# Performance work log

Measured on AMD Instinct MI355X. Metric: run time of the kernel, lower is better.

## Reference

```python
import jax, jax.numpy as jnp
import numpy as np


def setup_inputs() -> dict:
    key = jax.random.key(0)
    k1, k2 = jax.random.split(key)
    B, C, L, K = 128, 64, 4096, 31
    inputData = jax.random.normal(k1, (B, C, L), dtype=jnp.float32)
    # independentChannels=False: kernel = randn(1, C, K) expanded to (C, C, K)
    kernel = jnp.broadcast_to(jax.random.normal(k2, (1, C, K), dtype=jnp.float32), (C, C, K))
    return {"inputData": inputData, "kernel": kernel}


def reference(inputData, kernel):
    B, C, L = inputData.shape
    K = kernel.shape[-1]
    N = L + K - 1          # paddedSequenceLength
    pad = (K - 1) // 2
    # rfft with n=N zero-pads the last dim automatically (norm='backward' is jnp default)
    fourierData = jnp.fft.rfft(inputData, n=N, axis=-1)          # [B, C, N//2+1] complex
    kernelFFT = jnp.fft.rfft(kernel, n=N, axis=-1)               # [C, C, N//2+1] complex
    convFourier = jnp.einsum('oif,bif->bof', kernelFFT, fourierData)
    convData = jnp.fft.irfft(convFourier, n=N, axis=-1)          # [B, C, N]
    return convData[:, :, pad:N - pad]                           # [B, C, L]
```

## Files before the change

kernel.cpp:

```cpp
#include <hip/hip_runtime.h>

#define BATCH 128
#define C 64
#define L 4096
#define K 31

#define NT 512
#define NWAVE 8
#define CG 16
#define CPB (C / CG)
#define RW 8
#define WTILE 512

typedef float floatx4 __attribute__((ext_vector_type(4)));

__device__ __forceinline__ floatx4 ld4(const float* p) {
    return *reinterpret_cast<const floatx4*>(p);
}

#define KSTEP(k) { const float wk = wp[k];                              \
    P[(k)+0] += wk * o0.x; P[(k)+1] += wk * o0.y;                       \
    P[(k)+2] += wk * o0.z; P[(k)+3] += wk * o0.w;                       \
    P[(k)+4] += wk * o1.x; P[(k)+5] += wk * o1.y;                       \
    P[(k)+6] += wk * o1.z; P[(k)+7] += wk * o1.w; }

__global__ __launch_bounds__(NT, 2)
void computeS_kernel(const float* __restrict__ x,
                     const float* __restrict__ w,
                     float* __restrict__ Sp) {
    __shared__ float exL1[NWAVE][8];
    __shared__ float exL2a[NWAVE][8];
    __shared__ float exL2b[NWAVE][8];
    __shared__ float exR1[NWAVE][8];
    __shared__ float exR2a[NWAVE][8];
    __shared__ float exR2b[NWAVE][8];

    const int tid  = threadIdx.x;
    const int wv   = tid >> 6;
    const int lane = tid & 63;
    const int b    = blockIdx.x;
    const int cg   = blockIdx.y;
    const int l0   = wv * WTILE + lane * RW;
    const int i0   = cg * CPB;
    const float* xb = x + (long)b * C * L;

    float P[38] = {};

    const float* xi = xb + (long)i0 * L + l0;
    floatx4 o0 = ld4(xi), o1 = ld4(xi + 4);

    for (int c = 0; c < CPB; ++c) {
        floatx4 n0 = o0, n1 = o1;
        if (c + 1 < CPB) { n0 = ld4(xi + L); n1 = ld4(xi + L + 4); }

        const float* wp = w + (i0 + c) * K;
        KSTEP(0)  KSTEP(1)  KSTEP(2)  KSTEP(3)  KSTEP(4)  KSTEP(5)
        KSTEP(6)  KSTEP(7)  KSTEP(8)  KSTEP(9)  KSTEP(10) KSTEP(11)
        KSTEP(12) KSTEP(13) KSTEP(14) KSTEP(15) KSTEP(16) KSTEP(17)
        KSTEP(18) KSTEP(19) KSTEP(20) KSTEP(21) KSTEP(22) KSTEP(23)
        KSTEP(24) KSTEP(25) KSTEP(26) KSTEP(27) KSTEP(28) KSTEP(29)
        KSTEP(30)

        o0 = n0; o1 = n1;
        xi += L;
    }

    if (lane == 63) {
#pragma unroll
        for (int j = 0; j < 8; ++j) exL1[wv][j] = P[23 + j];
#pragma unroll
        for (int j = 0; j < 7; ++j) exL2b[wv][j] = P[31 + j];
    }
    if (lane == 62) {
#pragma unroll
        for (int j = 0; j < 7; ++j) exL2a[wv][j] = P[31 + j];
    }
    if (lane == 0) {
#pragma unroll
        for (int j = 0; j < 8; ++j) exR1[wv][j] = P[7 + j];
#pragma unroll
        for (int j = 0; j < 7; ++j) exR2b[wv][j] = P[j];
    }
    if (lane == 1) {
#pragma unroll
        for (int j = 0; j < 7; ++j) exR2a[wv][j] = P[j];
    }
    __syncthreads();

    float res[RW];
#pragma unroll
    for (int r = 0; r < RW; ++r) res[r] = P[15 + r];

#pragma unroll
    for (int r = 0; r < 8; ++r) {
        float v = __shfl_up(P[23 + r], 1, 64);
        if (lane == 0) v = (wv > 0) ? exL1[wv - 1][r] : 0.f;
        res[r] += v;
    }
#pragma unroll
    for (int r = 0; r < 7; ++r) {
        float v = __shfl_up(P[31 + r], 2, 64);
        if (lane == 0)      v = (wv > 0) ? exL2a[wv - 1][r] : 0.f;
        else if (lane == 1) v = (wv > 0) ? exL2b[wv - 1][r] : 0.f;
        res[r] += v;
    }
#pragma unroll
    for (int r = 0; r < 8; ++r) {
        float v = __shfl_down(P[7 + r], 1, 64);
        if (lane == 63) v = (wv < NWAVE - 1) ? exR1[wv + 1][r] : 0.f;
        res[r] += v;
    }
#pragma unroll
    for (int r = 1; r < 8; ++r) {
        float v = __shfl_down(P[r - 1], 2, 64);
        if (lane == 63)      v = (wv < NWAVE - 1) ? exR2a[wv + 1][r - 1] : 0.f;
        else if (lane == 62) v = (wv < NWAVE - 1) ? exR2b[wv + 1][r - 1] : 0.f;
        res[r] += v;
    }

    floatx4 s0, s1;
    s0.x = res[0]; s0.y = res[1]; s0.z = res[2]; s0.w = res[3];
    s1.x = res[4]; s1.y = res[5]; s1.z = res[6]; s1.w = res[7];
    float* sp = Sp + ((long)cg * BATCH + b) * L + l0;
    *reinterpret_cast<floatx4*>(sp)     = s0;
    *reinterpret_cast<floatx4*>(sp + 4) = s1;
}

__global__ __launch_bounds__(256)
void broadcast_kernel(const float* __restrict__ Sp,
                      float* __restrict__ out) {
    const int lane = threadIdx.x & 63;
    const int og   = threadIdx.x >> 6;
    const int b    = blockIdx.y;
    const int l4   = blockIdx.x * 64 + lane;
    const long sbase = (long)b * L + (long)l4 * 4;

    floatx4 v = *reinterpret_cast<const floatx4*>(Sp + sbase);
#pragma unroll
    for (int cg = 1; cg < CG; ++cg)
        v += *reinterpret_cast<const floatx4*>(Sp + (long)cg * BATCH * L + sbase);

    float* ob = out + ((long)b * C + og * 16) * L + (long)l4 * 4;
#pragma unroll
    for (int o = 0; o < 16; ++o)
        __builtin_nontemporal_store(v, reinterpret_cast<floatx4*>(ob + (long)o * L));
}

#define FB_R 4
#define FB_TILE (256 * FB_R)
#define FB_WIN 36
__global__ __launch_bounds__(256)
void fused_kernel(const float* __restrict__ x,
                  const float* __restrict__ w,
                  float* __restrict__ out) {
    const int tid = threadIdx.x;
    const int tile = blockIdx.x;
    const int b = blockIdx.y;
    const int l0 = tile * FB_TILE + tid * FB_R;
    float acc[FB_R] = {0.f, 0.f, 0.f, 0.f};
    const float* xb = x + (long)b * C * L;
    const bool interior = (l0 >= 16) && (l0 + 20 <= L);
    if (interior) {
        const float* xw = xb + (l0 - 16);
#pragma unroll 2
        for (int i = 0; i < C; ++i) {
            float win[FB_WIN];
            const floatx4* p = reinterpret_cast<const floatx4*>(xw + (long)i * L);
#pragma unroll
            for (int j = 0; j < FB_WIN / 4; ++j)
                reinterpret_cast<floatx4*>(win)[j] = p[j];
            const float* wp = w + i * K;
#pragma unroll
            for (int k = 0; k < K; ++k) {
                const float wk = wp[k];
#pragma unroll
                for (int r = 0; r < FB_R; ++r)
                    acc[r] += wk * win[r + 31 - k];
            }
        }
    } else {
        for (int i = 0; i < C; ++i) {
            const float* xi = xb + (long)i * L;
            float win[FB_WIN];
#pragma unroll
            for (int j = 0; j < FB_WIN; ++j) {
                const int g = l0 - 16 + j;
                win[j] = (g >= 0 && g < L) ? xi[g] : 0.f;
            }
            const float* wp = w + i * K;
#pragma unroll
            for (int k = 0; k < K; ++k) {
                const float wk = wp[k];
#pragma unroll
                for (int r = 0; r < FB_R; ++r)
                    acc[r] += wk * win[r + 31 - k];
            }
        }
    }
    float* op = out + (long)b * C * L + l0;
    floatx4 v; v.x = acc[0]; v.y = acc[1]; v.z = acc[2]; v.w = acc[3];
#pragma unroll
    for (int o = 0; o < C; ++o)
        __builtin_nontemporal_store(v, reinterpret_cast<floatx4*>(op + (long)o * L));
}

extern "C" void kernel_launch(void* const* d_in, const int* in_sizes, int n_in,
                              void* d_out, int out_size, void* d_ws, size_t ws_size,
                              hipStream_t stream) {
    const float* x = (const float*)d_in[0];
    const float* w = (const float*)d_in[1];
    float* out = (float*)d_out;

    const size_t sp_bytes = (size_t)CG * BATCH * L * sizeof(float);
    if (ws_size >= sp_bytes) {
        float* Sp = (float*)d_ws;
        dim3 grid1(BATCH, CG);
        computeS_kernel<<<grid1, NT, 0, stream>>>(x, w, Sp);
        dim3 grid2(L / 256, BATCH);
        broadcast_kernel<<<grid2, 256, 0, stream>>>(Sp, out);
    } else {
        dim3 grid(L / FB_TILE, BATCH);
        fused_kernel<<<grid, 256, 0, stream>>>(x, w, out);
    }
}
```

Before: 65.95 us.

## Fuse channel-sum and output broadcast into a single tiled reverse-conv kernel

Replaces the two-kernel path (partial sums written to workspace, then a reduce-and-broadcast kernel) with one kernel. Each block covers a 2048-wide sequence tile and splits the 64 input channels across two wave halves, reducing them through shared memory. Halo contributions at tile edges are computed by single lanes, and each wave writes 8 output channels straight from shared memory. This removes the workspace write/read round trip and one launch, at the cost of fewer blocks (256) and serial halo work on one lane.

```diff
diff --git a/kernel.cpp b/kernel.cpp
--- a/kernel.cpp
+++ b/kernel.cpp
@@ -7,10 +7,11 @@
 
 #define NT 512
 #define NWAVE 8
-#define CG 16
-#define CPB (C / CG)
+#define NWT 4
+#define CH 32
 #define RW 8
 #define WTILE 512
+#define BTILE 2048
 
 typedef float floatx4 __attribute__((ext_vector_type(4)));
 
@@ -25,23 +26,28 @@
     P[(k)+6] += wk * o1.z; P[(k)+7] += wk * o1.w; }
 
 __global__ __launch_bounds__(NT, 2)
-void computeS_kernel(const float* __restrict__ x,
-                     const float* __restrict__ w,
-                     float* __restrict__ Sp) {
+void revconv_fused(const float* __restrict__ x,
+                   const float* __restrict__ w,
+                   float* __restrict__ out) {
     __shared__ float exL1[NWAVE][8];
     __shared__ float exL2a[NWAVE][8];
     __shared__ float exL2b[NWAVE][8];
     __shared__ float exR1[NWAVE][8];
     __shared__ float exR2a[NWAVE][8];
     __shared__ float exR2b[NWAVE][8];
+    __shared__ __align__(16) float rbuf[BTILE];
+    __shared__ __align__(16) float sbuf[BTILE];
 
     const int tid  = threadIdx.x;
     const int wv   = tid >> 6;
     const int lane = tid & 63;
-    const int b    = blockIdx.x;
-    const int cg   = blockIdx.y;
-    const int l0   = wv * WTILE + lane * RW;
-    const int i0   = cg * CPB;
+    const int wt   = wv >> 1;
+    const int half = wv & 1;
+    const int tile = blockIdx.x;
+    const int b    = blockIdx.y;
+    const int T0   = tile * BTILE;
+    const int l0   = T0 + wt * WTILE + lane * RW;
+    const int i0   = half * CH;
     const float* xb = x + (long)b * C * L;
 
     float P[38] = {};
@@ -49,9 +55,9 @@
     const float* xi = xb + (long)i0 * L + l0;
     floatx4 o0 = ld4(xi), o1 = ld4(xi + 4);
 
-    for (int c = 0; c < CPB; ++c) {
+    for (int c = 0; c < CH; ++c) {
         floatx4 n0 = o0, n1 = o1;
-        if (c + 1 < CPB) { n0 = ld4(xi + L); n1 = ld4(xi + L + 4); }
+        if (c + 1 < CH) { n0 = ld4(xi + L); n1 = ld4(xi + L + 4); }
 
         const float* wp = w + (i0 + c) * K;
         KSTEP(0)  KSTEP(1)  KSTEP(2)  KSTEP(3)  KSTEP(4)  KSTEP(5)
@@ -65,6 +71,37 @@
         xi += L;
     }
 
+    if (wt == 0 && lane == 0 && tile > 0) {
+        for (int c = 0; c < CH; ++c) {
+            const float* gp = xb + (long)(i0 + c) * L + T0 - 16;
+            float g[16];
+#pragma unroll
+            for (int q = 0; q < 4; ++q)
+                *reinterpret_cast<floatx4*>(&g[q * 4]) = ld4(gp + q * 4);
+            const float* wp = w + (i0 + c) * K;
+#pragma unroll
+            for (int j = 1; j < 16; ++j)
+#pragma unroll
+                for (int k = 31 - j; k < 31; ++k)
+                    P[j + k - 16] += wp[k] * g[j];
+        }
+    }
+    if (wt == NWT - 1 && lane == 63 && tile == 0) {
+        for (int c = 0; c < CH; ++c) {
+            const float* gp = xb + (long)(i0 + c) * L + T0 + BTILE;
+            float g[16];
+#pragma unroll
+            for (int q = 0; q < 4; ++q)
+                *reinterpret_cast<floatx4*>(&g[q * 4]) = ld4(gp + q * 4);
+            const float* wp = w + (i0 + c) * K;
+#pragma unroll
+            for (int j = 0; j < 15; ++j)
+#pragma unroll
+                for (int k = 0; k <= 14 - j; ++k)
+                    P[j + k + 8] += wp[k] * g[j];
+        }
+    }
+
     if (lane == 63) {
 #pragma unroll
         for (int j = 0; j < 8; ++j) exL1[wv][j] = P[23 + j];
@@ -94,114 +131,61 @@
 #pragma unroll
     for (int r = 0; r < 8; ++r) {
         float v = __shfl_up(P[23 + r], 1, 64);
-        if (lane == 0) v = (wv > 0) ? exL1[wv - 1][r] : 0.f;
+        if (lane == 0) v = (wt > 0) ? exL1[wv - 2][r] : 0.f;
         res[r] += v;
     }
 #pragma unroll
     for (int r = 0; r < 7; ++r) {
         float v = __shfl_up(P[31 + r], 2, 64);
-        if (lane == 0)      v = (wv > 0) ? exL2a[wv - 1][r] : 0.f;
-        else if (lane == 1) v = (wv > 0) ? exL2b[wv - 1][r] : 0.f;
+        if (lane == 0)      v = (wt > 0) ? exL2a[wv - 2][r] : 0.f;
+        else if (lane == 1) v = (wt > 0) ? exL2b[wv - 2][r] : 0.f;
         res[r] += v;
     }
 #pragma unroll
     for (int r = 0; r < 8; ++r) {
         float v = __shfl_down(P[7 + r], 1, 64);
-        if (lane == 63) v = (wv < NWAVE - 1) ? exR1[wv + 1][r] : 0.f;
+        if (lane == 63) v = (wt < NWT - 1) ? exR1[wv + 2][r] : 0.f;
         res[r] += v;
     }
 #pragma unroll
     for (int r = 1; r < 8; ++r) {
         float v = __shfl_down(P[r - 1], 2, 64);
-        if (lane == 63)      v = (wv < NWAVE - 1) ? exR2a[wv + 1][r - 1] : 0.f;
-        else if (lane == 62) v = (wv < NWAVE - 1) ? exR2b[wv + 1][r - 1] : 0.f;
-        res[r] += v;
-    }
-
-    floatx4 s0, s1;
-    s0.x = res[0]; s0.y = res[1]; s0.z = res[2]; s0.w = res[3];
-    s1.x = res[4]; s1.y = res[5]; s1.z = res[6]; s1.w = res[7];
-    float* sp = Sp + ((long)cg * BATCH + b) * L + l0;
-    *reinterpret_cast<floatx4*>(sp)     = s0;
-    *reinterpret_cast<floatx4*>(sp + 4) = s1;
-}
-
-__global__ __launch_bounds__(256)
-void broadcast_kernel(const float* __restrict__ Sp,
-                      float* __restrict__ out) {
-    const int lane = threadIdx.x & 63;
-    const int og   = threadIdx.x >> 6;
-    const int b    = blockIdx.y;
-    const int l4   = blockIdx.x * 64 + lane;
-    const long sbase = (long)b * L + (long)l4 * 4;
-
-    floatx4 v = *reinterpret_cast<const floatx4*>(Sp + sbase);
-#pragma unroll
-    for (int cg = 1; cg < CG; ++cg)
-        v += *reinterpret_cast<const floatx4*>(Sp + (long)cg * BATCH * L + sbase);
-
-    float* ob = out + ((long)b * C + og * 16) * L + (long)l4 * 4;
-#pragma unroll
-    for (int o = 0; o < 16; ++o)
-        __builtin_nontemporal_store(v, reinterpret_cast<floatx4*>(ob + (long)o * L));
-}
-
-#define FB_R 4
-#define FB_TILE (256 * FB_R)
-#define FB_WIN 36
-__global__ __launch_bounds__(256)
-void fused_kernel(const float* __restrict__ x,
-                  const float* __restrict__ w,
-                  float* __restrict__ out) {
-    const int tid = threadIdx.x;
-    const int tile = blockIdx.x;
-    const int b = blockIdx.y;
-    const int l0 = tile * FB_TILE + tid * FB_R;
-    float acc[FB_R] = {0.f, 0.f, 0.f, 0.f};
-    const float* xb = x + (long)b * C * L;
-    const bool interior = (l0 >= 16) && (l0 + 20 <= L);
-    if (interior) {
-        const float* xw = xb + (l0 - 16);
-#pragma unroll 2
-        for (int i = 0; i < C; ++i) {
-            float win[FB_WIN];
-            const floatx4* p = reinterpret_cast<const floatx4*>(xw + (long)i * L);
-#pragma unroll
-            for (int j = 0; j < FB_WIN / 4; ++j)
-                reinterpret_cast<floatx4*>(win)[j] = p[j];
-            const float* wp = w + i * K;
-#pragma unroll
-            for (int k = 0; k < K; ++k) {
-                const float wk = wp[k];
-#pragma unroll
-                for (int r = 0; r < FB_R; ++r)
-                    acc[r] += wk * win[r + 31 - k];
-            }
+        if (lane == 63)      v = (wt < NWT - 1) ? exR2a[wv + 2][r - 1] : 0.f;
+        else if (lane == 62) v = (wt < NWT - 1) ? exR2b[wv + 2][r - 1] : 0.f;
+        res[r] += v;
+    }
+
+    const int toff = wt * WTILE + lane * RW;
+    if (half == 1) {
+        floatx4 a0, a1;
+        a0.x = res[0]; a0.y = res[1]; a0.z = res[2]; a0.w = res[3];
+        a1.x = res[4]; a1.y = res[5]; a1.z = res[6]; a1.w = res[7];
+        *reinterpret_cast<floatx4*>(&rbuf[toff])     = a0;
+        *reinterpret_cast<floatx4*>(&rbuf[toff + 4]) = a1;
+    }
+    __syncthreads();
+    if (half == 0) {
+        floatx4 s0, s1;
+        s0.x = res[0] + rbuf[toff];     s0.y = res[1] + rbuf[toff + 1];
+        s0.z = res[2] + rbuf[toff + 2]; s0.w = res[3] + rbuf[toff + 3];
+        s1.x = res[4] + rbuf[toff + 4]; s1.y = res[5] + rbuf[toff + 5];
+        s1.z = res[6] + rbuf[toff + 6]; s1.w = res[7] + rbuf[toff + 7];
+        *reinterpret_cast<floatx4*>(&sbuf[toff])     = s0;
+        *reinterpret_cast<floatx4*>(&sbuf[toff + 4]) = s1;
+    }
+    __syncthreads();
+
+    float* ob = out + ((long)b * C + wv * 8) * L + T0;
+#pragma unroll
+    for (int o = 0; o < 8; ++o) {
+        float* op = ob + (long)o * L;
+#pragma unroll
+        for (int q = 0; q < 8; ++q) {
+            const int idx4 = lane + q * 64;
+            const floatx4 v = ld4(&sbuf[idx4 * 4]);
+            __builtin_nontemporal_store(v, reinterpret_cast<floatx4*>(op + idx4 * 4));
         }
-    } else {
-        for (int i = 0; i < C; ++i) {
-            const float* xi = xb + (long)i * L;
-            float win[FB_WIN];
-#pragma unroll
-            for (int j = 0; j < FB_WIN; ++j) {
-                const int g = l0 - 16 + j;
-                win[j] = (g >= 0 && g < L) ? xi[g] : 0.f;
-            }
-            const float* wp = w + i * K;
-#pragma unroll
-            for (int k = 0; k < K; ++k) {
-                const float wk = wp[k];
-#pragma unroll
-                for (int r = 0; r < FB_R; ++r)
-                    acc[r] += wk * win[r + 31 - k];
-            }
-        }
-    }
-    float* op = out + (long)b * C * L + l0;
-    floatx4 v; v.x = acc[0]; v.y = acc[1]; v.z = acc[2]; v.w = acc[3];
-#pragma unroll
-    for (int o = 0; o < C; ++o)
-        __builtin_nontemporal_store(v, reinterpret_cast<floatx4*>(op + (long)o * L));
+    }
 }
 
 extern "C" void kernel_launch(void* const* d_in, const int* in_sizes, int n_in,
@@ -211,15 +195,6 @@
     const float* w = (const float*)d_in[1];
     float* out = (float*)d_out;
 
-    const size_t sp_bytes = (size_t)CG * BATCH * L * sizeof(float);
-    if (ws_size >= sp_bytes) {
-        float* Sp = (float*)d_ws;
-        dim3 grid1(BATCH, CG);
-        computeS_kernel<<<grid1, NT, 0, stream>>>(x, w, Sp);
-        dim3 grid2(L / 256, BATCH);
-        broadcast_kernel<<<grid2, 256, 0, stream>>>(Sp, out);
-    } else {
-        dim3 grid(L / FB_TILE, BATCH);
-        fused_kernel<<<grid, 256, 0, stream>>>(x, w, out);
-    }
+    dim3 grid(L / BTILE, BATCH);
+    revconv_fused<<<grid, NT, 0, stream>>>(x, w, out);
 }
```

Result: slower. 78.35 us (+18.8%).

## Fuse partial-sum and broadcast kernels via per-batch atomic counter spin-wait

Applied to the files above, without the earlier changes.

Merges the channel-partial-sum kernel and the broadcast kernel into one launch. Each batch's four channel-group blocks write partials, bump an atomic counter, spin until all four arrive, then each block reduces the partials and writes its quarter of the output channels. Channel groups drop from 16 to 4, so each block does more channels and the partial buffer shrinks. The change adds a memset launch, depends on all blocks of a batch being co-resident (deadlock risk under the spin-wait), and reduces parallelism in the compute phase.

```diff
diff --git a/kernel.cpp b/kernel.cpp
--- a/kernel.cpp
+++ b/kernel.cpp
@@ -7,10 +7,11 @@
 
 #define NT 512
 #define NWAVE 8
-#define CG 16
+#define CG 4
 #define CPB (C / CG)
 #define RW 8
 #define WTILE 512
+#define SP_FLOATS ((long)CG * BATCH * L)
 
 typedef float floatx4 __attribute__((ext_vector_type(4)));
 
@@ -24,10 +25,12 @@
     P[(k)+4] += wk * o1.x; P[(k)+5] += wk * o1.y;                       \
     P[(k)+6] += wk * o1.z; P[(k)+7] += wk * o1.w; }
 
-__global__ __launch_bounds__(NT, 2)
-void computeS_kernel(const float* __restrict__ x,
-                     const float* __restrict__ w,
-                     float* __restrict__ Sp) {
+__global__ __launch_bounds__(NT, 8)
+void revconv_persistent(const float* __restrict__ x,
+                        const float* __restrict__ w,
+                        float* __restrict__ Sp,
+                        int* __restrict__ done,
+                        float* __restrict__ out) {
     __shared__ float exL1[NWAVE][8];
     __shared__ float exL2a[NWAVE][8];
     __shared__ float exL2b[NWAVE][8];
@@ -38,8 +41,9 @@
     const int tid  = threadIdx.x;
     const int wv   = tid >> 6;
     const int lane = tid & 63;
-    const int b    = blockIdx.x;
-    const int cg   = blockIdx.y;
+    const int bid  = blockIdx.x;
+    const int b    = bid >> 2;
+    const int cg   = bid & 3;
     const int l0   = wv * WTILE + lane * RW;
     const int i0   = cg * CPB;
     const float* xb = x + (long)b * C * L;
@@ -118,32 +122,40 @@
         res[r] += v;
     }
 
-    floatx4 s0, s1;
-    s0.x = res[0]; s0.y = res[1]; s0.z = res[2]; s0.w = res[3];
-    s1.x = res[4]; s1.y = res[5]; s1.z = res[6]; s1.w = res[7];
-    float* sp = Sp + ((long)cg * BATCH + b) * L + l0;
-    *reinterpret_cast<floatx4*>(sp)     = s0;
-    *reinterpret_cast<floatx4*>(sp + 4) = s1;
-}
-
-__global__ __launch_bounds__(256)
-void broadcast_kernel(const float* __restrict__ Sp,
-                      float* __restrict__ out) {
-    const int lane = threadIdx.x & 63;
-    const int og   = threadIdx.x >> 6;
-    const int b    = blockIdx.y;
-    const int l4   = blockIdx.x * 64 + lane;
-    const long sbase = (long)b * L + (long)l4 * 4;
-
-    floatx4 v = *reinterpret_cast<const floatx4*>(Sp + sbase);
-#pragma unroll
-    for (int cg = 1; cg < CG; ++cg)
-        v += *reinterpret_cast<const floatx4*>(Sp + (long)cg * BATCH * L + sbase);
-
-    float* ob = out + ((long)b * C + og * 16) * L + (long)l4 * 4;
-#pragma unroll
-    for (int o = 0; o < 16; ++o)
-        __builtin_nontemporal_store(v, reinterpret_cast<floatx4*>(ob + (long)o * L));
+    {
+        floatx4 s0, s1;
+        s0.x = res[0]; s0.y = res[1]; s0.z = res[2]; s0.w = res[3];
+        s1.x = res[4]; s1.y = res[5]; s1.z = res[6]; s1.w = res[7];
+        float* sp = Sp + ((long)cg * BATCH + b) * L + l0;
+        *reinterpret_cast<floatx4*>(sp)     = s0;
+        *reinterpret_cast<floatx4*>(sp + 4) = s1;
+    }
+
+    __syncthreads();
+    if (tid == 0)
+        __hip_atomic_fetch_add(&done[b], 1, __ATOMIC_RELEASE, __HIP_MEMORY_SCOPE_AGENT);
+
+    if (tid == 0) {
+        while (__hip_atomic_load(&done[b], __ATOMIC_ACQUIRE, __HIP_MEMORY_SCOPE_AGENT) < CG)
+            __builtin_amdgcn_s_sleep(1);
+    }
+    __syncthreads();
+
+    floatx4 va = 0.f, vb = 0.f;
+#pragma unroll
+    for (int p = 0; p < CG; ++p) {
+        const float* pp = Sp + ((long)p * BATCH + b) * L + tid * 4;
+        va += ld4(pp);
+        vb += ld4(pp + 2048);
+    }
+
+    float* ob = out + ((long)b * C + cg * CPB) * L;
+#pragma unroll
+    for (int o = 0; o < CPB; ++o) {
+        float* op = ob + (long)o * L + tid * 4;
+        __builtin_nontemporal_store(va, reinterpret_cast<floatx4*>(op));
+        __builtin_nontemporal_store(vb, reinterpret_cast<floatx4*>(op + 2048));
+    }
 }
 
 #define FB_R 4
@@ -211,13 +223,13 @@
     const float* w = (const float*)d_in[1];
     float* out = (float*)d_out;
 
-    const size_t sp_bytes = (size_t)CG * BATCH * L * sizeof(float);
-    if (ws_size >= sp_bytes) {
-        float* Sp = (float*)d_ws;
-        dim3 grid1(BATCH, CG);
-        computeS_kernel<<<grid1, NT, 0, stream>>>(x, w, Sp);
-        dim3 grid2(L / 256, BATCH);
-        broadcast_kernel<<<grid2, 256, 0, stream>>>(Sp, out);
+    const size_t sp_bytes = SP_FLOATS * sizeof(float);
+    const size_t need = sp_bytes + BATCH * sizeof(int);
+    if (ws_size >= need) {
+        float* Sp  = (float*)d_ws;
+        int* done  = (int*)((char*)d_ws + sp_bytes);
+        hipMemsetAsync(done, 0, BATCH * sizeof(int), stream);
+        revconv_persistent<<<BATCH * CG, NT, 0, stream>>>(x, w, Sp, done, out);
     } else {
         dim3 grid(L / FB_TILE, BATCH);
         fused_kernel<<<grid, 256, 0, stream>>>(x, w, out);
```

New measurement: 97.76 us. +48.2%, slower.
